# Kernel optimization log

Hardware: AMD Instinct MI355X
Metric: run time of the kernel (lower is better)

Reference implementation:

```python
import jax, jax.numpy as jnp
import numpy as np
from jax.scipy.special import erfinv

N_CHUNKS = 64
D = 128          # input_dim
O = 256          # output_dim
B = 4096         # batch (batch_last)
P = D // 2       # number of 2D pairs

def get_borders_cdf_grid(n):
    # CDF (Gaussian-quantile) spaced grid borders; clip probs to keep endpoints finite
    p = jnp.clip(jnp.arange(n + 1, dtype=jnp.float32) / n, 0.5 / n, 1.0 - 0.5 / n)
    return jnp.sqrt(2.0) * erfinv(2.0 * p - 1.0)

BORDERS = get_borders_cdf_grid(N_CHUNKS)  # (n_chunks+1,)


def setup_inputs() -> dict:
    key = jax.random.key(0)
    ks = jax.random.split(key, 5)
    s = 1.0 / np.sqrt(D)
    return {
        "x": jax.random.normal(ks[0], (D, B), dtype=jnp.float32),
        "weight_lmKAN": jnp.ones((1,), dtype=jnp.float32),
        "apply_relu_linear": 1,
        "func_parameter": jax.random.uniform(ks[1], (N_CHUNKS + 1, N_CHUNKS + 1, O, P), minval=-s, maxval=s, dtype=jnp.float32),
        "scale_parameters": jnp.ones((D,), dtype=jnp.float32),
        "bias_parameters": jnp.zeros((D,), dtype=jnp.float32),
        "W_linear": jax.random.uniform(ks[2], (O, D), minval=-s, maxval=s, dtype=jnp.float32),
        "bias_linear": jax.random.uniform(ks[3], (O,), minval=-s, maxval=s, dtype=jnp.float32),
    }


def lmkan_2d(fp, x):
    """2D bucketized grid lookup + bilinear interpolation.
    fp: (G, G, O, P) with G = n_chunks+1; x: (D, B) -> out (O, B)."""
    n = fp.shape[0] - 1
    pairs = x.reshape(P, 2, -1)                      # adjacent-channel pairs
    eps = 1e-6
    x1 = jnp.clip(pairs[:, 0], BORDERS[0], BORDERS[-1] - eps)  # (P, B)
    x2 = jnp.clip(pairs[:, 1], BORDERS[0], BORDERS[-1] - eps)
    i = jnp.clip(jnp.searchsorted(BORDERS, x1, side='right') - 1, 0, n - 1)
    j = jnp.clip(jnp.searchsorted(BORDERS, x2, side='right') - 1, 0, n - 1)
    t1 = (x1 - BORDERS[i]) / (BORDERS[i + 1] - BORDERS[i])      # (P, B) in [0,1)
    t2 = (x2 - BORDERS[j]) / (BORDERS[j + 1] - BORDERS[j])
    pidx = jnp.arange(P)[:, None]                    # (P, 1) -> broadcasts to (P, B)

    def corner(ii, jj, w):
        g = fp[ii, jj, :, pidx]                      # gather -> (P, B, O)
        return jnp.einsum('pb,pbo->ob', w, g)

    return (corner(i,     j,     (1.0 - t1) * (1.0 - t2))
          + corner(i + 1, j,     t1 * (1.0 - t2))
          + corner(i,     j + 1, (1.0 - t1) * t2)
          + corner(i + 1, j + 1, t1 * t2))


def reference(x, weight_lmKAN, apply_relu_linear, func_parameter, scale_parameters, bias_parameters, W_linear, bias_linear):
    # relu_last=True branch of the original forward
    linear_out = W_linear @ x + bias_linear[:, None]         # (O, B)
    if apply_relu_linear:
        linear_out = jax.nn.relu(linear_out)
    xs = x * scale_parameters[:, None] + bias_parameters[:, None]  # apply_scale / apply_bias
    # apply_tanh=False
    lmkan_out = lmkan_2d(func_parameter, xs)                 # (O, B)
    return 1.0 * linear_out + weight_lmKAN * lmkan_out
```

## Files before the change

### kernel.cpp

```cpp
#include <hip/hip_runtime.h>
#include <hip/hip_fp16.h>


#define NB 4096
#define ND 128
#define NO 256
#define NP 64
#define NG 65
#define PANEL 16384

typedef float f32x4 __attribute__((ext_vector_type(4)));
union Pack8 { __half h[8]; uint4 v; };

__device__ __forceinline__ int bsearch65(const float* B, float v) {
  int lo = 0, hi = 65;
  while (lo < hi) {
    int m = (lo + hi) >> 1;
    if (B[m] <= v) lo = m + 1; else hi = m;
  }
  int i = lo - 1;
  return i < 0 ? 0 : (i > 63 ? 63 : i);
}

__global__ __launch_bounds__(256) void lmkan_transpose3(
    const float* __restrict__ src, __half* __restrict__ dst) {
  const int panel = blockIdx.x;
  const int t = threadIdx.x;
  __shared__ __half lds[256 * 72];

  const f32x4* s4 = reinterpret_cast<const f32x4*>(src + (size_t)panel * PANEL);
#pragma unroll
  for (int k = 0; k < 16; ++k) {
    int idx4 = t + 256 * k;
    f32x4 v = __builtin_nontemporal_load(&s4[idx4]);
    int o = idx4 >> 4;
    int p0 = (idx4 & 15) * 4;
    int p0s = p0 ^ (((o >> 3) & 15) << 2);
    union { __half2 h2[2]; uint2 u; } pk;
    pk.h2[0] = __floats2half2_rn(v[0], v[1]);
    pk.h2[1] = __floats2half2_rn(v[2], v[3]);
    *reinterpret_cast<uint2*>(&lds[o * 72 + p0s]) = pk.u;
  }
  __syncthreads();

  const int l = t & 63, w = t >> 6;
  const int o0 = (l & 31) * 8;
  const int swz = (l & 15) << 2;
#pragma unroll
  for (int ss = 0; ss < 8; ++ss) {
    int p = ss * 8 + w * 2 + (l >> 5);
    int prow = ((p & ~3) ^ swz) + (p & 3);
    Pack8 pk;
#pragma unroll
    for (int r = 0; r < 8; ++r) pk.h[r] = lds[(o0 + r) * 72 + prow];
    *reinterpret_cast<uint4*>(dst + ((size_t)panel * 64 + p) * NO + o0) = pk.v;
  }
}

__device__ __forceinline__ void fma4h(float acc[4], float w, uint2 v) {
  __half2 h0 = *reinterpret_cast<__half2*>(&v.x);
  __half2 h1 = *reinterpret_cast<__half2*>(&v.y);
  float2 f0 = __half22float2(h0);
  float2 f1 = __half22float2(h1);
  acc[0] = fmaf(w, f0.x, acc[0]);
  acc[1] = fmaf(w, f0.y, acc[1]);
  acc[2] = fmaf(w, f1.x, acc[2]);
  acc[3] = fmaf(w, f1.y, acc[3]);
}

__global__ __launch_bounds__(256) void lmkan_gather5(
    const float* __restrict__ x, const float* __restrict__ scale,
    const float* __restrict__ biasp, const float* __restrict__ wlm_p,
    const __half* __restrict__ fpt, float* __restrict__ out) {
  const int b = blockIdx.x;
  const int t = threadIdx.x;
  const int w = t >> 6;
  const int l = t & 63;

  __shared__ float borders[66];
  __shared__ float xcol[ND];
  __shared__ int pbaseEl[NP];
  __shared__ float4 pw[NP];
  __shared__ __align__(16) float lm[4][NO];

  if (t < 65) {
    float pk = fminf(fmaxf((float)t * (1.0f / 64.0f), 0.0078125f), 0.9921875f);
    borders[t] = 1.41421356237309515f * erfinvf(2.0f * pk - 1.0f);
  }
  if (t < ND) xcol[t] = x[(size_t)t * NB + b];
  __syncthreads();

  if (t < NP) {
    const int p = t;
    float x1 = xcol[2 * p]     * scale[2 * p]     + biasp[2 * p];
    float x2 = xcol[2 * p + 1] * scale[2 * p + 1] + biasp[2 * p + 1];
    const float lo = borders[0];
    const float hi = borders[64] - 1e-6f;
    x1 = fminf(fmaxf(x1, lo), hi);
    x2 = fminf(fmaxf(x2, lo), hi);
    int i = bsearch65(borders, x1);
    int j = bsearch65(borders, x2);
    float t1 = (x1 - borders[i]) / (borders[i + 1] - borders[i]);
    float t2 = (x2 - borders[j]) / (borders[j + 1] - borders[j]);
    pbaseEl[p] = ((i * NG + j) * 64 + p) * NO;
    pw[p] = make_float4((1.0f - t1) * (1.0f - t2),
                        (1.0f - t1) * t2,
                        t1 * (1.0f - t2),
                        t1 * t2);
  }
  __syncthreads();

  float acc[4] = {0, 0, 0, 0};
  const int p0 = w * 16;
  const int loff = 4 * l;

  const __half* q = fpt + pbaseEl[p0] + loff;
  uint2 vA = *reinterpret_cast<const uint2*>(q);
  uint2 vB = *reinterpret_cast<const uint2*>(q + PANEL);
  uint2 vC = *reinterpret_cast<const uint2*>(q + 65 * PANEL);
  uint2 vD = *reinterpret_cast<const uint2*>(q + 66 * PANEL);
#pragma unroll
  for (int pi = 0; pi < 16; ++pi) {
    const int p = p0 + pi;
    uint2 cA = vA, cB = vB, cC = vC, cD = vD;
    if (pi < 15) {
      const __half* qn = fpt + pbaseEl[p + 1] + loff;
      vA = *reinterpret_cast<const uint2*>(qn);
      vB = *reinterpret_cast<const uint2*>(qn + PANEL);
      vC = *reinterpret_cast<const uint2*>(qn + 65 * PANEL);
      vD = *reinterpret_cast<const uint2*>(qn + 66 * PANEL);
    }
    const float4 wv = pw[p];
    fma4h(acc, wv.x, cA);
    fma4h(acc, wv.y, cB);
    fma4h(acc, wv.z, cC);
    fma4h(acc, wv.w, cD);
  }
  *reinterpret_cast<float4*>(&lm[w][loff]) =
      make_float4(acc[0], acc[1], acc[2], acc[3]);
  __syncthreads();

  const int o = t;
  float lmsum = lm[0][o] + lm[1][o] + lm[2][o] + lm[3][o];
  out[(size_t)o * NB + b] = wlm_p[0] * lmsum;
}

__global__ __launch_bounds__(256) void lmkan_linear(
    const float* __restrict__ x, const float* __restrict__ W,
    const float* __restrict__ bias_l, const int* __restrict__ relu_p,
    float* __restrict__ out) {
  const int b0 = blockIdx.x * 32;
  const int t = threadIdx.x;
  __shared__ __align__(16) float xs[32 * 132];

#pragma unroll
  for (int k = 0; k < 16; ++k) {
    int idx = t + 256 * k;
    int d = idx >> 5, bb = idx & 31;
    xs[bb * 132 + d] = x[(size_t)d * NB + b0 + bb];
  }
  __syncthreads();

  float acc[32];
#pragma unroll
  for (int bb = 0; bb < 32; ++bb) acc[bb] = 0.0f;

  const float4* W4 = reinterpret_cast<const float4*>(W + (size_t)t * ND);
#pragma unroll 8
  for (int d4 = 0; d4 < 32; ++d4) {
    float4 wv = W4[d4];
#pragma unroll
    for (int bb = 0; bb < 32; ++bb) {
      float4 xv = *reinterpret_cast<const float4*>(&xs[bb * 132 + d4 * 4]);
      acc[bb] = fmaf(wv.x, xv.x, acc[bb]);
      acc[bb] = fmaf(wv.y, xv.y, acc[bb]);
      acc[bb] = fmaf(wv.z, xv.z, acc[bb]);
      acc[bb] = fmaf(wv.w, xv.w, acc[bb]);
    }
  }

  const float bias = bias_l[t];
  const int rl = relu_p[0];
  float* orow = out + (size_t)t * NB + b0;
#pragma unroll
  for (int bb = 0; bb < 32; ++bb) {
    float v = acc[bb] + bias;
    if (rl) v = fmaxf(v, 0.0f);
    orow[bb] += v;
  }
}

__global__ __launch_bounds__(64) void lmkan_gather_direct(
    const float* __restrict__ x, const float* __restrict__ scale,
    const float* __restrict__ biasp, const float* __restrict__ W,
    const float* __restrict__ bias_l, const float* __restrict__ wlm_p,
    const int* __restrict__ relu_p, const float* __restrict__ fp,
    float* __restrict__ out) {
  const int b = blockIdx.x;
  const int t = threadIdx.x;

  __shared__ float borders[66];
  __shared__ __align__(16) float xcol[ND];
  __shared__ int pbase[NP];
  __shared__ float4 pw[NP];

  for (int k = t; k < 65; k += 64) {
    float pk = fminf(fmaxf((float)k * (1.0f / 64.0f), 0.0078125f), 0.9921875f);
    borders[k] = 1.41421356237309515f * erfinvf(2.0f * pk - 1.0f);
  }
  xcol[t]      = x[(size_t)t * NB + b];
  xcol[t + 64] = x[(size_t)(t + 64) * NB + b];
  __syncthreads();

  {
    const int p = t;
    float x1 = xcol[2 * p]     * scale[2 * p]     + biasp[2 * p];
    float x2 = xcol[2 * p + 1] * scale[2 * p + 1] + biasp[2 * p + 1];
    const float lo = borders[0];
    const float hi = borders[64] - 1e-6f;
    x1 = fminf(fmaxf(x1, lo), hi);
    x2 = fminf(fmaxf(x2, lo), hi);
    int i = bsearch65(borders, x1);
    int j = bsearch65(borders, x2);
    float t1 = (x1 - borders[i]) / (borders[i + 1] - borders[i]);
    float t2 = (x2 - borders[j]) / (borders[j + 1] - borders[j]);
    pbase[p] = i * NG + j;
    pw[p] = make_float4((1.0f - t1) * (1.0f - t2), t1 * (1.0f - t2),
                        (1.0f - t1) * t2, t1 * t2);
  }
  __syncthreads();

  float acc[4] = {0, 0, 0, 0};
  for (int p = 0; p < NP; ++p) {
    int base = pbase[p];
    float4 wv = pw[p];
#pragma unroll
    for (int k = 0; k < 4; ++k) {
      size_t r = ((size_t)base * NO + (4 * t + k)) * NP + p;
      acc[k] += wv.x * fp[r] + wv.y * fp[r + 65 * PANEL] +
                wv.z * fp[r + PANEL] + wv.w * fp[r + 66 * PANEL];
    }
  }

  const float wlm = wlm_p[0];
  const int rl = relu_p[0];
  const float4* xc4 = reinterpret_cast<const float4*>(xcol);
#pragma unroll
  for (int k = 0; k < 4; ++k) {
    const int o = 4 * t + k;
    const float4* wr = reinterpret_cast<const float4*>(W + (size_t)o * ND);
    float s = 0.0f;
#pragma unroll 8
    for (int d4 = 0; d4 < ND / 4; ++d4) {
      float4 wv = wr[d4];
      float4 xv = xc4[d4];
      s = fmaf(wv.x, xv.x, s);
      s = fmaf(wv.y, xv.y, s);
      s = fmaf(wv.z, xv.z, s);
      s = fmaf(wv.w, xv.w, s);
    }
    s += bias_l[o];
    if (rl) s = fmaxf(s, 0.0f);
    out[(size_t)o * NB + b] = s + wlm * acc[k];
  }
}

extern "C" void kernel_launch(void* const* d_in, const int* in_sizes, int n_in,
                              void* d_out, int out_size, void* d_ws, size_t ws_size,
                              hipStream_t stream) {
  const float* x     = reinterpret_cast<const float*>(d_in[0]);
  const float* wlm   = reinterpret_cast<const float*>(d_in[1]);
  const int*   relu  = reinterpret_cast<const int*>(d_in[2]);
  const float* fp    = reinterpret_cast<const float*>(d_in[3]);
  const float* scale = reinterpret_cast<const float*>(d_in[4]);
  const float* biasp = reinterpret_cast<const float*>(d_in[5]);
  const float* W     = reinterpret_cast<const float*>(d_in[6]);
  const float* bl    = reinterpret_cast<const float*>(d_in[7]);
  float* out = reinterpret_cast<float*>(d_out);

  const size_t need = (size_t)NG * NG * PANEL * sizeof(__half);
  if (ws_size >= need) {
    __half* fpt = reinterpret_cast<__half*>(d_ws);
    lmkan_transpose3<<<NG * NG, 256, 0, stream>>>(fp, fpt);
    lmkan_gather5<<<NB, 256, 0, stream>>>(x, scale, biasp, wlm, fpt, out);
    lmkan_linear<<<NB / 32, 256, 0, stream>>>(x, W, bl, relu, out);
  } else {
    lmkan_gather_direct<<<NB, 64, 0, stream>>>(x, scale, biasp, W, bl, wlm, relu, fp, out);
  }
}
```

Baseline: 182.4 us.

## Partition gather by pair groups per XCD and reduce partials in linear kernel

The gather kernel is restructured so each block handles 16 batch columns and one group of 8 pairs. The pair group is picked from the block index modulo 8, which appears intended to map to XCDs so each XCD's L2 only sees one eighth of the transposed table. Each block writes partial sums for its group into a workspace buffer, and the linear kernel reduces the 8 partials and combines them with the linear output. This trades better L2 locality for the cost of writing and reading a partials buffer (4096×8×256 floats) and extra block syncs per pair.

```diff
diff --git a/kernel.cpp b/kernel.cpp
--- a/kernel.cpp
+++ b/kernel.cpp
@@ -8,6 +8,9 @@
 #define NP 64
 #define NG 65
 #define PANEL 16384
+#define FPT_ELEMS ((size_t)NG * NG * PANEL)
+#define FPT_BYTES (FPT_ELEMS * 2)
+#define PART_FLOATS ((size_t)NB * 8 * NO)
 
 typedef float f32x4 __attribute__((ext_vector_type(4)));
 union Pack8 { __half h[8]; uint4 v; };
@@ -20,6 +23,13 @@
   }
   int i = lo - 1;
   return i < 0 ? 0 : (i > 63 ? 63 : i);
+}
+
+__device__ __forceinline__ void borders_init(float* borders, int t) {
+  if (t < 65) {
+    float pk = fminf(fmaxf((float)t * (1.0f / 64.0f), 0.0078125f), 0.9921875f);
+    borders[t] = 1.41421356237309515f * erfinvf(2.0f * pk - 1.0f);
+  }
 }
 
 __global__ __launch_bounds__(256) void lmkan_transpose3(
@@ -68,86 +78,77 @@
   acc[3] = fmaf(w, f1.y, acc[3]);
 }
 
-__global__ __launch_bounds__(256) void lmkan_gather5(
+__global__ __launch_bounds__(128, 4) void lmkan_gather6(
     const float* __restrict__ x, const float* __restrict__ scale,
-    const float* __restrict__ biasp, const float* __restrict__ wlm_p,
-    const __half* __restrict__ fpt, float* __restrict__ out) {
-  const int b = blockIdx.x;
+    const float* __restrict__ biasp, const __half* __restrict__ fpt,
+    float* __restrict__ part) {
+  const int xcd = blockIdx.x & 7;
+  const int m   = blockIdx.x >> 3;
   const int t = threadIdx.x;
   const int w = t >> 6;
   const int l = t & 63;
 
   __shared__ float borders[66];
-  __shared__ float xcol[ND];
-  __shared__ int pbaseEl[NP];
-  __shared__ float4 pw[NP];
-  __shared__ __align__(16) float lm[4][NO];
-
-  if (t < 65) {
-    float pk = fminf(fmaxf((float)t * (1.0f / 64.0f), 0.0078125f), 0.9921875f);
-    borders[t] = 1.41421356237309515f * erfinvf(2.0f * pk - 1.0f);
-  }
-  if (t < ND) xcol[t] = x[(size_t)t * NB + b];
-  __syncthreads();
-
-  if (t < NP) {
-    const int p = t;
-    float x1 = xcol[2 * p]     * scale[2 * p]     + biasp[2 * p];
-    float x2 = xcol[2 * p + 1] * scale[2 * p + 1] + biasp[2 * p + 1];
-    const float lo = borders[0];
-    const float hi = borders[64] - 1e-6f;
-    x1 = fminf(fmaxf(x1, lo), hi);
-    x2 = fminf(fmaxf(x2, lo), hi);
-    int i = bsearch65(borders, x1);
-    int j = bsearch65(borders, x2);
-    float t1 = (x1 - borders[i]) / (borders[i + 1] - borders[i]);
-    float t2 = (x2 - borders[j]) / (borders[j + 1] - borders[j]);
-    pbaseEl[p] = ((i * NG + j) * 64 + p) * NO;
-    pw[p] = make_float4((1.0f - t1) * (1.0f - t2),
-                        (1.0f - t1) * t2,
-                        t1 * (1.0f - t2),
-                        t1 * t2);
-  }
-  __syncthreads();
-
-  float acc[4] = {0, 0, 0, 0};
-  const int p0 = w * 16;
+  __shared__ int jb[16];
+  __shared__ float4 w4[16];
+
+  borders_init(borders, t);
+  __syncthreads();
+
+  float acc[8][4] = {};
   const int loff = 4 * l;
 
-  const __half* q = fpt + pbaseEl[p0] + loff;
-  uint2 vA = *reinterpret_cast<const uint2*>(q);
-  uint2 vB = *reinterpret_cast<const uint2*>(q + PANEL);
-  uint2 vC = *reinterpret_cast<const uint2*>(q + 65 * PANEL);
-  uint2 vD = *reinterpret_cast<const uint2*>(q + 66 * PANEL);
-#pragma unroll
-  for (int pi = 0; pi < 16; ++pi) {
-    const int p = p0 + pi;
-    uint2 cA = vA, cB = vB, cC = vC, cD = vD;
-    if (pi < 15) {
-      const __half* qn = fpt + pbaseEl[p + 1] + loff;
-      vA = *reinterpret_cast<const uint2*>(qn);
-      vB = *reinterpret_cast<const uint2*>(qn + PANEL);
-      vC = *reinterpret_cast<const uint2*>(qn + 65 * PANEL);
-      vD = *reinterpret_cast<const uint2*>(qn + 66 * PANEL);
-    }
-    const float4 wv = pw[p];
-    fma4h(acc, wv.x, cA);
-    fma4h(acc, wv.y, cB);
-    fma4h(acc, wv.z, cC);
-    fma4h(acc, wv.w, cD);
-  }
-  *reinterpret_cast<float4*>(&lm[w][loff]) =
-      make_float4(acc[0], acc[1], acc[2], acc[3]);
-  __syncthreads();
-
-  const int o = t;
-  float lmsum = lm[0][o] + lm[1][o] + lm[2][o] + lm[3][o];
-  out[(size_t)o * NB + b] = wlm_p[0] * lmsum;
-}
-
-__global__ __launch_bounds__(256) void lmkan_linear(
+#pragma unroll
+  for (int ph = 0; ph < 8; ++ph) {
+    const int p = 8 * xcd + ph;
+    if (t < 16) {
+      const int b = m * 16 + t;
+      float x1 = x[(size_t)(2 * p) * NB + b]     * scale[2 * p]     + biasp[2 * p];
+      float x2 = x[(size_t)(2 * p + 1) * NB + b] * scale[2 * p + 1] + biasp[2 * p + 1];
+      const float lo = borders[0];
+      const float hi = borders[64] - 1e-6f;
+      x1 = fminf(fmaxf(x1, lo), hi);
+      x2 = fminf(fmaxf(x2, lo), hi);
+      int i = bsearch65(borders, x1);
+      int j = bsearch65(borders, x2);
+      float t1 = (x1 - borders[i]) / (borders[i + 1] - borders[i]);
+      float t2 = (x2 - borders[j]) / (borders[j + 1] - borders[j]);
+      jb[t] = ((i * NG + j) * 64 + p) * NO;
+      w4[t] = make_float4((1.0f - t1) * (1.0f - t2),
+                          (1.0f - t1) * t2,
+                          t1 * (1.0f - t2),
+                          t1 * t2);
+    }
+    __syncthreads();
+#pragma unroll
+    for (int bb = 0; bb < 8; ++bb) {
+      const int bl = w * 8 + bb;
+      const float4 wv = w4[bl];
+      const __half* q = fpt + jb[bl] + loff;
+      uint2 vA = *reinterpret_cast<const uint2*>(q);
+      uint2 vB = *reinterpret_cast<const uint2*>(q + PANEL);
+      uint2 vC = *reinterpret_cast<const uint2*>(q + 65 * PANEL);
+      uint2 vD = *reinterpret_cast<const uint2*>(q + 66 * PANEL);
+      fma4h(acc[bb], wv.x, vA);
+      fma4h(acc[bb], wv.y, vB);
+      fma4h(acc[bb], wv.z, vC);
+      fma4h(acc[bb], wv.w, vD);
+    }
+    __syncthreads();
+  }
+
+#pragma unroll
+  for (int bb = 0; bb < 8; ++bb) {
+    const int b = m * 16 + w * 8 + bb;
+    *reinterpret_cast<float4*>(&part[((size_t)b * 8 + xcd) * NO + loff]) =
+        make_float4(acc[bb][0], acc[bb][1], acc[bb][2], acc[bb][3]);
+  }
+}
+
+__global__ __launch_bounds__(256) void lmkan_linear2(
     const float* __restrict__ x, const float* __restrict__ W,
     const float* __restrict__ bias_l, const int* __restrict__ relu_p,
+    const float* __restrict__ wlm_p, const float* __restrict__ part,
     float* __restrict__ out) {
   const int b0 = blockIdx.x * 32;
   const int t = threadIdx.x;
@@ -181,12 +182,17 @@
 
   const float bias = bias_l[t];
   const int rl = relu_p[0];
+  const float wlm = wlm_p[0];
   float* orow = out + (size_t)t * NB + b0;
-#pragma unroll
+#pragma unroll 4
   for (int bb = 0; bb < 32; ++bb) {
+    float lmsum = 0.0f;
+    const float* pr = part + ((size_t)(b0 + bb) * 8) * NO + t;
+#pragma unroll
+    for (int k = 0; k < 8; ++k) lmsum += pr[k * NO];
     float v = acc[bb] + bias;
     if (rl) v = fmaxf(v, 0.0f);
-    orow[bb] += v;
+    orow[bb] = v + wlm * lmsum;
   }
 }
 
@@ -278,12 +284,14 @@
   const float* bl    = reinterpret_cast<const float*>(d_in[7]);
   float* out = reinterpret_cast<float*>(d_out);
 
-  const size_t need = (size_t)NG * NG * PANEL * sizeof(__half);
+  const size_t need = FPT_BYTES + PART_FLOATS * sizeof(float);
   if (ws_size >= need) {
     __half* fpt = reinterpret_cast<__half*>(d_ws);
+    float* part = reinterpret_cast<float*>(
+        reinterpret_cast<char*>(d_ws) + FPT_BYTES);
     lmkan_transpose3<<<NG * NG, 256, 0, stream>>>(fp, fpt);
-    lmkan_gather5<<<NB, 256, 0, stream>>>(x, scale, biasp, wlm, fpt, out);
-    lmkan_linear<<<NB / 32, 256, 0, stream>>>(x, W, bl, relu, out);
+    lmkan_gather6<<<2048, 128, 0, stream>>>(x, scale, biasp, fpt, part);
+    lmkan_linear2<<<NB / 32, 256, 0, stream>>>(x, W, bl, relu, wlm, part, out);
   } else {
     lmkan_gather_direct<<<NB, 64, 0, stream>>>(x, scale, biasp, W, bl, wlm, relu, fp, out);
   }
```

Result: slower. 486.1 us (+166.5%).
